# Performance work log

Hardware: AMD Instinct MI355X
Metric: run time of the kernel (lower is better)

Reference implementation:

```python
import jax, jax.numpy as jnp
import numpy as np

B, C, H, W = 2, 256, 64, 64
NH = 4          # num_heads -> ch = C // NH = 64
G = 32          # GroupNorm groups (normalization(channels))
EPS = 1e-5


def setup_inputs() -> dict:
    key = jax.random.key(0)
    ks = jax.random.split(key, 7)
    s = 1.0 / np.sqrt(C).astype(np.float32)
    return {
        "x": jax.random.normal(ks[0], (B, C, H, W), jnp.float32),
        "gn_scale": 1.0 + 0.02 * jax.random.normal(ks[1], (C,), jnp.float32),
        "gn_bias": 0.02 * jax.random.normal(ks[2], (C,), jnp.float32),
        "w_qkv": s * jax.random.normal(ks[3], (3 * C, C), jnp.float32),
        "b_qkv": jnp.zeros((3 * C,), jnp.float32),
        # NOTE: original zero-inits proj_out; we use random weights so the
        # attention path contributes to the output (meaningful baseline).
        "w_proj": s * jax.random.normal(ks[4], (C, C), jnp.float32),
        "b_proj": jnp.zeros((C,), jnp.float32),
    }


def reference(x, gn_scale, gn_bias, w_qkv, b_qkv, w_proj, b_proj):
    b, c = x.shape[0], x.shape[1]
    spatial = x.shape[2:]
    t = int(np.prod(spatial))
    xf = x.reshape(b, c, t)                      # [B, C, T]

    # GroupNorm(32) over (channels-in-group, T)
    xg = xf.reshape(b, G, c // G, t)
    mu = xg.mean(axis=(2, 3), keepdims=True)
    var = xg.var(axis=(2, 3), keepdims=True)
    xn = ((xg - mu) * jax.lax.rsqrt(var + EPS)).reshape(b, c, t)
    xn = xn * gn_scale[None, :, None] + gn_bias[None, :, None]

    # 1x1 conv -> qkv: [B, 3C, T]
    qkv = jnp.einsum('oc,bct->bot', w_qkv, xn) + b_qkv[None, :, None]

    # QKVAttentionLegacy: reshape (B*H, 3*ch, T) then split
    ch = c // NH
    qkv_h = qkv.reshape(b * NH, 3 * ch, t)
    q, k, v = jnp.split(qkv_h, 3, axis=1)        # each [B*H, ch, T]
    scale = 1.0 / np.sqrt(np.sqrt(ch)).astype(np.float32)
    w = jnp.einsum('bct,bcs->bts', q * scale, k * scale)   # [B*H, T, T]
    w = jax.nn.softmax(w.astype(jnp.float32), axis=-1).astype(qkv.dtype)
    a = jnp.einsum('bts,bcs->bct', w, v).reshape(b, c, t)  # [B, C, T]

    # proj 1x1 conv + residual
    h = jnp.einsum('oc,bct->bot', w_proj, a) + b_proj[None, :, None]
    return (xf + h).reshape(b, c, *spatial)
```

## Files before the change

### kernel.cpp

```cpp
#include <hip/hip_runtime.h>
#include <math.h>

#define T 4096
#define C 256
#define BATCH 2
#define NH 4
#define G 32
#define CPG 8
#define EPS 1e-5f
#define LOG2E 1.4426950408889634f
#define QSCALE (0.125f * LOG2E)
#define KSPLIT 4
#define KRANGE (T / KSPLIT)
#define KTILE 128
#define NIT (KRANGE / KTILE)
#define BH (BATCH * NH)

typedef __attribute__((ext_vector_type(8))) short bfv8;
typedef __attribute__((ext_vector_type(4))) short bfv4;
typedef __attribute__((ext_vector_type(4))) float f32x4;
typedef __attribute__((ext_vector_type(2))) float f32x2;
typedef __attribute__((ext_vector_type(16))) float f32x16;

static __device__ __forceinline__ short f2bf(float f) {
    union { float f; unsigned u; } v; v.f = f;
    return (short)((v.u + 0x7FFFu + ((v.u >> 16) & 1u)) >> 16);
}
static __device__ __forceinline__ float bf2f(short s) {
    union { float f; unsigned u; } v; v.u = ((unsigned)(unsigned short)s) << 16;
    return v.f;
}

#if __has_builtin(__builtin_amdgcn_exp2f)
#define EXP2(x) __builtin_amdgcn_exp2f(x)
#else
#define EXP2(x) exp2f(x)
#endif

#define AS1 __attribute__((address_space(1)))
#define AS3 __attribute__((address_space(3)))
static __device__ __forceinline__ void gll16(const void* g, void* l) {
    __builtin_amdgcn_global_load_lds((const AS1 void*)g, (AS3 void*)l, 16, 0, 0);
}

__global__ __launch_bounds__(256) void prep_stats(
    const float* __restrict__ wq, const float* __restrict__ wp,
    short* __restrict__ wqb, short* __restrict__ wpb,
    const float* __restrict__ x, float* __restrict__ gnp)
{
    __shared__ float rs[256], rss[256];
    const int bid = blockIdx.x;
    const int tid = threadIdx.x;
    if (bid < 256) {
        int i = bid * 256 + tid;
        const int NQ = 768 * 256 / 4;
        float4 v; short* dst;
        if (i < NQ) { v = ((const float4*)wq)[i]; dst = wqb + i * 4; }
        else        { int j = i - NQ; v = ((const float4*)wp)[j]; dst = wpb + j * 4; }
        bfv4 o = { f2bf(v.x), f2bf(v.y), f2bf(v.z), f2bf(v.w) };
        *(bfv4*)dst = o;
        return;
    }
    const int blk = (bid - 256) >> 2;
    const int ts  = (bid - 256) & 3;
    const int b = blk / G, g = blk % G;
    const float* xp = x + ((size_t)b * C + g * CPG) * T + ts * 1024;

    float s = 0.f, ss = 0.f;
    #pragma unroll
    for (int u = 0; u < CPG; u++) {
        float4 v = ((const float4*)(xp + (size_t)u * T))[tid];
        s  += v.x + v.y + v.z + v.w;
        ss += v.x*v.x + v.y*v.y + v.z*v.z + v.w*v.w;
    }
    rs[tid] = s; rss[tid] = ss;
    __syncthreads();
    for (int off = 128; off > 0; off >>= 1) {
        if (tid < off) { rs[tid] += rs[tid+off]; rss[tid] += rss[tid+off]; }
        __syncthreads();
    }
    if (tid == 0) {
        gnp[(blk * 4 + ts) * 2 + 0] = rs[0];
        gnp[(blk * 4 + ts) * 2 + 1] = rss[0];
    }
}

__global__ __launch_bounds__(256) void gn_norm(const float* __restrict__ x,
                                               const float* __restrict__ scale,
                                               const float* __restrict__ bias,
                                               const float* __restrict__ gnp,
                                               short* __restrict__ xnT) {
    const int blk = blockIdx.x;
    const int ts  = blockIdx.y;
    const int b = blk / G, g = blk % G;
    const int c0 = g * CPG;
    const float* xp = x + ((size_t)b * C + c0) * T;

    float s = 0.f, ss = 0.f;
    #pragma unroll
    for (int i = 0; i < 4; i++) {
        s  += gnp[(blk * 4 + i) * 2 + 0];
        ss += gnp[(blk * 4 + i) * 2 + 1];
    }
    const float inv_n = 1.0f / (CPG * T);
    const float mu  = s * inv_n;
    const float var = ss * inv_n - mu * mu;
    const float rstd = rsqrtf(var + EPS);

    float sc[CPG], bi[CPG];
    #pragma unroll
    for (int u = 0; u < CPG; u++) {
        sc[u] = scale[c0+u] * rstd;
        bi[u] = bias[c0+u] - mu * sc[u];
    }

    const int t = ts * 1024 + threadIdx.x * 4;
    float vv[CPG][4];
    #pragma unroll
    for (int u = 0; u < CPG; u++) {
        float4 v = *(const float4*)&xp[(size_t)u * T + t];
        vv[u][0] = v.x * sc[u] + bi[u];
        vv[u][1] = v.y * sc[u] + bi[u];
        vv[u][2] = v.z * sc[u] + bi[u];
        vv[u][3] = v.w * sc[u] + bi[u];
    }
    #pragma unroll
    for (int j = 0; j < 4; j++) {
        bfv8 w = { f2bf(vv[0][j]), f2bf(vv[1][j]), f2bf(vv[2][j]), f2bf(vv[3][j]),
                   f2bf(vv[4][j]), f2bf(vv[5][j]), f2bf(vv[6][j]), f2bf(vv[7][j]) };
        *(bfv8*)&xnT[((size_t)b * T + t + j) * C + c0] = w;
    }
}

__global__ __launch_bounds__(256) void gemm_qkv(
    const short* __restrict__ wq,
    const float* __restrict__ bq,
    const short* __restrict__ xnT,
    short* __restrict__ qb, short* __restrict__ kb, short* __restrict__ vb)
{
    const int b  = blockIdx.z;
    const int t0 = blockIdx.x * 64;
    const int ot = blockIdx.y;
    const int h = ot / 3, part = ot % 3;
    const int o0 = ot * 64;

    __shared__ short sm[8192];
    short* Ab = sm;
    short* Bb = sm + 4096;

    const int tid = threadIdx.x, lane = tid & 63, wave = tid >> 6;
    const int col = lane & 15, quad = lane >> 4;
    const short* xb = xnT + (size_t)b * T * C;

    f32x4 acc[4];
    #pragma unroll
    for (int g = 0; g < 4; g++) { acc[g][0]=0.f; acc[g][1]=0.f; acc[g][2]=0.f; acc[g][3]=0.f; }

    for (int k0 = 0; k0 < C; k0 += 64) {
        __syncthreads();
        #pragma unroll
        for (int hh = 0; hh < 2; hh++) {
            gll16(wq + (size_t)(o0 + 16*wave + col) * C + k0 + hh*32 + quad*8,
                  Ab + (hh*4 + wave) * 512);
            gll16(xb + (size_t)(t0 + 16*wave + col) * C + k0 + hh*32 + quad*8,
                  Bb + (hh*4 + wave) * 512);
        }
        __syncthreads();
        #pragma unroll
        for (int hh = 0; hh < 2; hh++) {
            bfv8 af = *(const bfv8*)(Ab + (hh*4 + wave) * 512 + lane*8);
            #pragma unroll
            for (int g = 0; g < 4; g++) {
                bfv8 bf = *(const bfv8*)(Bb + (hh*4 + g) * 512 + lane*8);
                acc[g] = __builtin_amdgcn_mfma_f32_16x16x32_bf16(af, bf, acc[g], 0, 0, 0);
            }
        }
    }

    const int olocal = 16*wave + quad*4;
    float bias_r[4];
    #pragma unroll
    for (int r = 0; r < 4; r++) bias_r[r] = bq[o0 + olocal + r];
    const size_t hd = (size_t)(b * NH + h);

    if (part < 2) {
        short* dst = (part == 0 ? qb : kb) + hd * T * 64;
        const float sc = (part == 0) ? QSCALE : 1.0f;
        #pragma unroll
        for (int g = 0; g < 4; g++) {
            int t = t0 + 16*g + col;
            bfv4 w = { f2bf((acc[g][0] + bias_r[0]) * sc),
                       f2bf((acc[g][1] + bias_r[1]) * sc),
                       f2bf((acc[g][2] + bias_r[2]) * sc),
                       f2bf((acc[g][3] + bias_r[3]) * sc) };
            *(bfv4*)&dst[(size_t)t * 64 + olocal] = w;
        }
    } else {
        short* dst = vb + hd * 64 * T;
        const int pcol = (col & 3) | ((col & 4) << 1) | ((col & 8) >> 1);
        #pragma unroll
        for (int g = 0; g < 4; g++)
            #pragma unroll
            for (int r = 0; r < 4; r++)
                dst[(size_t)(olocal + r) * T + t0 + 16*g + pcol] =
                    f2bf(acc[g][r] + bias_r[r]);
    }
}

__global__ __launch_bounds__(512, 4) void attn_kernel(
    const short* __restrict__ qb,
    const short* __restrict__ kb,
    const short* __restrict__ vb,
    short* __restrict__ opart,
    float* __restrict__ lp)
{
    __shared__ short smem[32768];
    const int flat = blockIdx.x;
    const int bh = flat & 7;
    const int tb = (flat >> 3) & 15;
    const int ks = flat >> 7;
    const int t0 = tb * 256;
    const int k0base = ks * KRANGE;
    const short* kbh = kb + (size_t)bh * T * 64;
    const short* vbh = vb + (size_t)bh * 64 * T;

    const int tid  = threadIdx.x;
    const int lane = tid & 63;
    const int wave = tid >> 6;
    const int klow = lane & 31;
    const int hi   = lane >> 5;

    const int q = t0 + wave*32 + klow;
    const short* qrow = qb + (size_t)bh * T * 64 + (size_t)q * 64;
    bfv8 qf[4];
    #pragma unroll
    for (int s = 0; s < 4; s++) qf[s] = *(const bfv8*)(qrow + s*16 + hi*8);

    f32x16 oacc[2];
    #pragma unroll
    for (int c = 0; c < 2; c++)
        #pragma unroll
        for (int r = 0; r < 16; r++) oacc[c][r] = 0.f;
    f32x2 l2 = { 0.f, 0.f };

    const int n1 = tid, n2 = tid + 512;
    const int kOff1 = ((n1>>8)*32 + (n1&31))*64 + ((n1>>6)&3)*16 + ((n1>>5)&1)*8;
    const int kOff2 = ((n2>>8)*32 + (n2&31))*64 + ((n2>>6)&3)*16 + ((n2>>5)&1)*8;
    const size_t vRow1 = (size_t)(((n1>>9)<<5) + (n1&31)) * T;
    const size_t vRow2 = (size_t)(((n2>>9)<<5) + (n2&31)) * T;
    const int vCol1 = ((n1>>6)&7)*16 + ((n1>>5)&1)*8;
    const int vCol2 = ((n2>>6)&7)*16 + ((n2>>5)&1)*8;
    #define STAGE_KV(buf, s0)                                                   \
        {                                                                       \
            short* base = smem + (buf) * 16384;                                 \
            gll16(kbh + (size_t)(s0) * 64 + kOff1, base + n1*8);                \
            gll16(kbh + (size_t)(s0) * 64 + kOff2, base + n2*8);                \
            gll16(vbh + vRow1 + (s0) + vCol1, base + 8192 + n1*8);              \
            gll16(vbh + vRow2 + (s0) + vCol2, base + 8192 + n2*8);              \
        }

    STAGE_KV(0, k0base)

    for (int it = 0; it < NIT; it++) {
        __syncthreads();
        if (it + 1 < NIT) STAGE_KV((it+1) & 1, k0base + (it+1)*KTILE)

        const short* kvb = smem + (it & 1) * 16384;

        #pragma unroll
        for (int kt = 0; kt < 4; kt++) {
            f32x16 sacc;
            #pragma unroll
            for (int r = 0; r < 16; r++) sacc[r] = 0.f;
            #pragma unroll
            for (int s = 0; s < 4; s++) {
                bfv8 kf = *(const bfv8*)(kvb + ((kt*4 + s)*64 + lane)*8);
                sacc = __builtin_amdgcn_mfma_f32_32x32x16_bf16(kf, qf[s], sacc, 0, 0, 0);
            }
            #pragma unroll
            for (int u = 0; u < 2; u++) {
                float p[8];
                #pragma unroll
                for (int j = 0; j < 8; j++) p[j] = EXP2(sacc[8*u + j]);
                f32x2 pa = { p[0], p[1] }, pb = { p[2], p[3] };
                f32x2 pc = { p[4], p[5] }, pd = { p[6], p[7] };
                l2 += (pa + pb) + (pc + pd);
                union { unsigned w[4]; bfv8 v; } pk_;
                #pragma unroll
                for (int w = 0; w < 4; w++)
                    asm("v_cvt_pk_bf16_f32 %0, %1, %2"
                        : "=v"(pk_.w[w]) : "v"(p[2*w]), "v"(p[2*w+1]));
                const int kc = 2*kt + u;
                #pragma unroll
                for (int c = 0; c < 2; c++) {
                    bfv8 vf = *(const bfv8*)(kvb + 8192 + ((c*8 + kc)*64 + lane)*8);
                    oacc[c] = __builtin_amdgcn_mfma_f32_32x32x16_bf16(
                                  vf, pk_.v, oacc[c], 0, 0, 0);
                }
            }
        }
    }

    float lsum = l2[0] + l2[1];
    lsum += __shfl_xor(lsum, 32);

    const size_t rowbase = (size_t)(ks*BH + bh) * T + t0 + wave*32;
    short* opb = opart + (rowbase + klow) * 64;
    #pragma unroll
    for (int c = 0; c < 2; c++)
        #pragma unroll
        for (int u = 0; u < 4; u++) {
            bfv4 w = { f2bf(oacc[c][4*u+0]), f2bf(oacc[c][4*u+1]),
                       f2bf(oacc[c][4*u+2]), f2bf(oacc[c][4*u+3]) };
            *(bfv4*)(opb + c*32 + u*8 + hi*4) = w;
        }
    if (hi == 0) {
        lp[rowbase + klow] = lsum;
    }
}

__global__ __launch_bounds__(256) void gemm_proj(
    const short* __restrict__ wp,
    const float* __restrict__ bp,
    const short* __restrict__ opart,
    const float* __restrict__ lp,
    const float* __restrict__ x,
    float* __restrict__ out)
{
    const int b  = blockIdx.z;
    const int t0 = blockIdx.x * 64;
    const int o0 = blockIdx.y * 64;

    __shared__ short sm[8192];
    short* Ab = sm;
    short* Bb = sm + 4096;

    const int tid = threadIdx.x, lane = tid & 63, wave = tid >> 6;
    const int col = lane & 15, quad = lane >> 4;

    const int trow = t0 + 16*wave + col;
    float rl4[NH];
    #pragma unroll
    for (int hh = 0; hh < NH; hh++) {
        float ls = 0.f;
        #pragma unroll
        for (int ks = 0; ks < KSPLIT; ks++)
            ls += lp[((size_t)(ks*BH) + b*NH + hh) * T + trow];
        rl4[hh] = 1.0f / ls;
    }

    f32x4 acc[4];
    #pragma unroll
    for (int g = 0; g < 4; g++) { acc[g][0]=0.f; acc[g][1]=0.f; acc[g][2]=0.f; acc[g][3]=0.f; }

    for (int k0 = 0; k0 < C; k0 += 64) {
        __syncthreads();
        #pragma unroll
        for (int hh = 0; hh < 2; hh++) {
            gll16(wp + (size_t)(o0 + 16*wave + col) * C + k0 + hh*32 + quad*8,
                  Ab + (hh*4 + wave) * 512);
            const int chg = k0 + hh*32 + quad*8;
            const int hd = chg >> 6, chin = chg & 63;
            const short* ob = opart + (((size_t)(b*NH + hd)) * T + trow) * 64 + chin;
            float a8[8] = {0.f,0.f,0.f,0.f,0.f,0.f,0.f,0.f};
            #pragma unroll
            for (int ks = 0; ks < KSPLIT; ks++) {
                bfv8 v = *(const bfv8*)(ob + (size_t)ks * BH * T * 64);
                #pragma unroll
                for (int u = 0; u < 8; u++) a8[u] += bf2f(v[u]);
            }
            const float rl = rl4[hd];
            bfv8 pk;
            #pragma unroll
            for (int u = 0; u < 8; u++) pk[u] = f2bf(a8[u] * rl);
            *(bfv8*)(Bb + (hh*4 + wave) * 512 + lane*8) = pk;
        }
        __syncthreads();
        #pragma unroll
        for (int hh = 0; hh < 2; hh++) {
            bfv8 af = *(const bfv8*)(Ab + (hh*4 + wave) * 512 + lane*8);
            #pragma unroll
            for (int g = 0; g < 4; g++) {
                bfv8 bf = *(const bfv8*)(Bb + (hh*4 + g) * 512 + lane*8);
                acc[g] = __builtin_amdgcn_mfma_f32_16x16x32_bf16(af, bf, acc[g], 0, 0, 0);
            }
        }
    }

    const int olocal = 16*wave + quad*4;
    #pragma unroll
    for (int r = 0; r < 4; r++) {
        const int o = o0 + olocal + r;
        const float bias = bp[o];
        const size_t rowoff = ((size_t)b * C + o) * T;
        #pragma unroll
        for (int g = 0; g < 4; g++) {
            const size_t idx = rowoff + t0 + 16*g + col;
            out[idx] = acc[g][r] + bias + x[idx];
        }
    }
}

extern "C" void kernel_launch(void* const* d_in, const int* in_sizes, int n_in,
                              void* d_out, int out_size, void* d_ws, size_t ws_size,
                              hipStream_t stream) {
    (void)in_sizes; (void)n_in; (void)out_size; (void)ws_size;
    const float* x        = (const float*)d_in[0];
    const float* gn_scale = (const float*)d_in[1];
    const float* gn_bias  = (const float*)d_in[2];
    const float* w_qkv    = (const float*)d_in[3];
    const float* b_qkv    = (const float*)d_in[4];
    const float* w_proj   = (const float*)d_in[5];
    const float* b_proj   = (const float*)d_in[6];
    float* out = (float*)d_out;

    short* ws    = (short*)d_ws;
    short* qb    = ws;
    short* kb    = qb  + (size_t)BH * T * 64;
    short* vb    = kb  + (size_t)BH * T * 64;
    short* xnT   = vb  + (size_t)BH * T * 64;
    short* wqb   = xnT + (size_t)BATCH * T * C;
    short* wpb   = wqb + 768 * 256;
    short* opart = wpb + 256 * 256;
    float* lp    = (float*)(opart + (size_t)KSPLIT * BH * T * 64);
    float* gnp   = lp + (size_t)KSPLIT * BH * T;

    prep_stats<<<dim3(512), 256, 0, stream>>>(w_qkv, w_proj, wqb, wpb, x, gnp);
    gn_norm<<<dim3(BATCH * G, 4), 256, 0, stream>>>(x, gn_scale, gn_bias, gnp, xnT);
    gemm_qkv<<<dim3(T/64, 12, BATCH), 256, 0, stream>>>(wqb, b_qkv, xnT, qb, kb, vb);
    attn_kernel<<<dim3(512), 512, 0, stream>>>(qb, kb, vb, opart, lp);
    gemm_proj<<<dim3(T/64, 4, BATCH), 256, 0, stream>>>(wpb, b_proj, opart, lp, x, out);
}
```

Measured before the change: 146.8 us.

## Give each attention wave two query tiles to reuse K/V fragments

The attention kernel moves from 8 waves of 32 queries each to 4 waves of 64 queries each. Each wave now holds two query tiles, so every K and V fragment read from LDS feeds two MFMAs instead of one. The KV tile shrinks to 64 keys and LDS use is halved. The aim is to cut LDS read traffic per MFMA, at the cost of doubled accumulator registers, a lower occupancy bound, and more barrier iterations per block.

Measured after the change: 146.6 us. No clear change (-0.1%).

```diff
diff --git a/kernel.cpp b/kernel.cpp
--- a/kernel.cpp
+++ b/kernel.cpp
@@ -12,7 +12,7 @@
 #define QSCALE (0.125f * LOG2E)
 #define KSPLIT 4
 #define KRANGE (T / KSPLIT)
-#define KTILE 128
+#define KTILE 64
 #define NIT (KRANGE / KTILE)
 #define BH (BATCH * NH)
 
@@ -207,14 +207,14 @@
     }
 }
 
-__global__ __launch_bounds__(512, 4) void attn_kernel(
+__global__ __launch_bounds__(256, 2) void attn_kernel(
     const short* __restrict__ qb,
     const short* __restrict__ kb,
     const short* __restrict__ vb,
     short* __restrict__ opart,
     float* __restrict__ lp)
 {
-    __shared__ short smem[32768];
+    __shared__ short smem[16384];
     const int flat = blockIdx.x;
     const int bh = flat & 7;
     const int tb = (flat >> 3) & 15;
@@ -230,33 +230,37 @@
     const int klow = lane & 31;
     const int hi   = lane >> 5;
 
-    const int q = t0 + wave*32 + klow;
-    const short* qrow = qb + (size_t)bh * T * 64 + (size_t)q * 64;
-    bfv8 qf[4];
-    #pragma unroll
-    for (int s = 0; s < 4; s++) qf[s] = *(const bfv8*)(qrow + s*16 + hi*8);
-
-    f32x16 oacc[2];
+    const short* qrowA = qb + (size_t)bh * T * 64
+                            + (size_t)(t0 + wave*64 + klow) * 64;
+    const short* qrowB = qrowA + (size_t)32 * 64;
+    bfv8 qfA[4], qfB[4];
+    #pragma unroll
+    for (int s = 0; s < 4; s++) {
+        qfA[s] = *(const bfv8*)(qrowA + s*16 + hi*8);
+        qfB[s] = *(const bfv8*)(qrowB + s*16 + hi*8);
+    }
+
+    f32x16 oaccA[2], oaccB[2];
     #pragma unroll
     for (int c = 0; c < 2; c++)
         #pragma unroll
-        for (int r = 0; r < 16; r++) oacc[c][r] = 0.f;
-    f32x2 l2 = { 0.f, 0.f };
-
-    const int n1 = tid, n2 = tid + 512;
+        for (int r = 0; r < 16; r++) { oaccA[c][r] = 0.f; oaccB[c][r] = 0.f; }
+    f32x2 l2A = { 0.f, 0.f }, l2B = { 0.f, 0.f };
+
+    const int n1 = tid, n2 = tid + 256;
     const int kOff1 = ((n1>>8)*32 + (n1&31))*64 + ((n1>>6)&3)*16 + ((n1>>5)&1)*8;
     const int kOff2 = ((n2>>8)*32 + (n2&31))*64 + ((n2>>6)&3)*16 + ((n2>>5)&1)*8;
-    const size_t vRow1 = (size_t)(((n1>>9)<<5) + (n1&31)) * T;
-    const size_t vRow2 = (size_t)(((n2>>9)<<5) + (n2&31)) * T;
-    const int vCol1 = ((n1>>6)&7)*16 + ((n1>>5)&1)*8;
-    const int vCol2 = ((n2>>6)&7)*16 + ((n2>>5)&1)*8;
+    const size_t vRow1 = (size_t)((n1>>8)*32 + (n1&31)) * T;
+    const size_t vRow2 = (size_t)((n2>>8)*32 + (n2&31)) * T;
+    const int vCol1 = ((n1>>6)&3)*16 + ((n1>>5)&1)*8;
+    const int vCol2 = ((n2>>6)&3)*16 + ((n2>>5)&1)*8;
     #define STAGE_KV(buf, s0)                                                   \
         {                                                                       \
-            short* base = smem + (buf) * 16384;                                 \
+            short* base = smem + (buf) * 8192;                                  \
             gll16(kbh + (size_t)(s0) * 64 + kOff1, base + n1*8);                \
             gll16(kbh + (size_t)(s0) * 64 + kOff2, base + n2*8);                \
-            gll16(vbh + vRow1 + (s0) + vCol1, base + 8192 + n1*8);              \
-            gll16(vbh + vRow2 + (s0) + vCol2, base + 8192 + n2*8);              \
+            gll16(vbh + vRow1 + (s0) + vCol1, base + 4096 + n1*8);              \
+            gll16(vbh + vRow2 + (s0) + vCol2, base + 4096 + n2*8);              \
         }
 
     STAGE_KV(0, k0base)
@@ -265,57 +269,76 @@
         __syncthreads();
         if (it + 1 < NIT) STAGE_KV((it+1) & 1, k0base + (it+1)*KTILE)
 
-        const short* kvb = smem + (it & 1) * 16384;
-
-        #pragma unroll
-        for (int kt = 0; kt < 4; kt++) {
-            f32x16 sacc;
-            #pragma unroll
-            for (int r = 0; r < 16; r++) sacc[r] = 0.f;
+        const short* kvb = smem + (it & 1) * 8192;
+
+        #pragma unroll
+        for (int kt = 0; kt < 2; kt++) {
+            f32x16 sA, sB;
+            #pragma unroll
+            for (int r = 0; r < 16; r++) { sA[r] = 0.f; sB[r] = 0.f; }
             #pragma unroll
             for (int s = 0; s < 4; s++) {
                 bfv8 kf = *(const bfv8*)(kvb + ((kt*4 + s)*64 + lane)*8);
-                sacc = __builtin_amdgcn_mfma_f32_32x32x16_bf16(kf, qf[s], sacc, 0, 0, 0);
+                sA = __builtin_amdgcn_mfma_f32_32x32x16_bf16(kf, qfA[s], sA, 0, 0, 0);
+                sB = __builtin_amdgcn_mfma_f32_32x32x16_bf16(kf, qfB[s], sB, 0, 0, 0);
             }
             #pragma unroll
             for (int u = 0; u < 2; u++) {
-                float p[8];
+                float pA[8], pB[8];
                 #pragma unroll
-                for (int j = 0; j < 8; j++) p[j] = EXP2(sacc[8*u + j]);
-                f32x2 pa = { p[0], p[1] }, pb = { p[2], p[3] };
-                f32x2 pc = { p[4], p[5] }, pd = { p[6], p[7] };
-                l2 += (pa + pb) + (pc + pd);
-                union { unsigned w[4]; bfv8 v; } pk_;
+                for (int j = 0; j < 8; j++) {
+                    pA[j] = EXP2(sA[8*u + j]);
+                    pB[j] = EXP2(sB[8*u + j]);
+                }
+                f32x2 a0 = { pA[0], pA[1] }, a1 = { pA[2], pA[3] };
+                f32x2 a2 = { pA[4], pA[5] }, a3 = { pA[6], pA[7] };
+                l2A += (a0 + a1) + (a2 + a3);
+                f32x2 b0 = { pB[0], pB[1] }, b1 = { pB[2], pB[3] };
+                f32x2 b2 = { pB[4], pB[5] }, b3 = { pB[6], pB[7] };
+                l2B += (b0 + b1) + (b2 + b3);
+                union { unsigned w[4]; bfv8 v; } pkA_, pkB_;
                 #pragma unroll
-                for (int w = 0; w < 4; w++)
+                for (int w = 0; w < 4; w++) {
                     asm("v_cvt_pk_bf16_f32 %0, %1, %2"
-                        : "=v"(pk_.w[w]) : "v"(p[2*w]), "v"(p[2*w+1]));
+                        : "=v"(pkA_.w[w]) : "v"(pA[2*w]), "v"(pA[2*w+1]));
+                    asm("v_cvt_pk_bf16_f32 %0, %1, %2"
+                        : "=v"(pkB_.w[w]) : "v"(pB[2*w]), "v"(pB[2*w+1]));
+                }
                 const int kc = 2*kt + u;
                 #pragma unroll
                 for (int c = 0; c < 2; c++) {
-                    bfv8 vf = *(const bfv8*)(kvb + 8192 + ((c*8 + kc)*64 + lane)*8);
-                    oacc[c] = __builtin_amdgcn_mfma_f32_32x32x16_bf16(
-                                  vf, pk_.v, oacc[c], 0, 0, 0);
+                    bfv8 vf = *(const bfv8*)(kvb + 4096 + ((c*4 + kc)*64 + lane)*8);
+                    oaccA[c] = __builtin_amdgcn_mfma_f32_32x32x16_bf16(
+                                   vf, pkA_.v, oaccA[c], 0, 0, 0);
+                    oaccB[c] = __builtin_amdgcn_mfma_f32_32x32x16_bf16(
+                                   vf, pkB_.v, oaccB[c], 0, 0, 0);
                 }
             }
         }
     }
 
-    float lsum = l2[0] + l2[1];
-    lsum += __shfl_xor(lsum, 32);
-
-    const size_t rowbase = (size_t)(ks*BH + bh) * T + t0 + wave*32;
-    short* opb = opart + (rowbase + klow) * 64;
+    float lsumA = l2A[0] + l2A[1];
+    float lsumB = l2B[0] + l2B[1];
+    lsumA += __shfl_xor(lsumA, 32);
+    lsumB += __shfl_xor(lsumB, 32);
+
+    const size_t rowbase = (size_t)(ks*BH + bh) * T + t0 + wave*64;
+    short* opbA = opart + (rowbase + klow) * 64;
+    short* opbB = opart + (rowbase + 32 + klow) * 64;
     #pragma unroll
     for (int c = 0; c < 2; c++)
         #pragma unroll
         for (int u = 0; u < 4; u++) {
-            bfv4 w = { f2bf(oacc[c][4*u+0]), f2bf(oacc[c][4*u+1]),
-                       f2bf(oacc[c][4*u+2]), f2bf(oacc[c][4*u+3]) };
-            *(bfv4*)(opb + c*32 + u*8 + hi*4) = w;
+            bfv4 wA = { f2bf(oaccA[c][4*u+0]), f2bf(oaccA[c][4*u+1]),
+                        f2bf(oaccA[c][4*u+2]), f2bf(oaccA[c][4*u+3]) };
+            *(bfv4*)(opbA + c*32 + u*8 + hi*4) = wA;
+            bfv4 wB = { f2bf(oaccB[c][4*u+0]), f2bf(oaccB[c][4*u+1]),
+                        f2bf(oaccB[c][4*u+2]), f2bf(oaccB[c][4*u+3]) };
+            *(bfv4*)(opbB + c*32 + u*8 + hi*4) = wB;
         }
     if (hi == 0) {
-        lp[rowbase + klow] = lsum;
+        lp[rowbase + klow] = lsumA;
+        lp[rowbase + 32 + klow] = lsumB;
     }
 }
 
@@ -428,6 +451,6 @@
     prep_stats<<<dim3(512), 256, 0, stream>>>(w_qkv, w_proj, wqb, wpb, x, gnp);
     gn_norm<<<dim3(BATCH * G, 4), 256, 0, stream>>>(x, gn_scale, gn_bias, gnp, xnT);
     gemm_qkv<<<dim3(T/64, 12, BATCH), 256, 0, stream>>>(wqb, b_qkv, xnT, qb, kb, vb);
-    attn_kernel<<<dim3(512), 512, 0, stream>>>(qb, kb, vb, opart, lp);
+    attn_kernel<<<dim3(512), 256, 0, stream>>>(qb, kb, vb, opart, lp);
     gemm_proj<<<dim3(T/64, 4, BATCH), 256, 0, stream>>>(wpb, b_proj, opart, lp, x, out);
 }
```

## Load K/V fragments directly from global memory instead of LDS double-buffering

Applied to the files above, without the earlier changes.

Drops the shared-memory double-buffered staging of K and V tiles (async global-to-LDS loads plus a block barrier per tile) in the attention kernel. Each wave now reads its K and V MFMA fragments straight from global memory and relies on the L1/L2 caches for reuse across the block's eight waves. It also relaxes the launch bounds from a minimum of 4 blocks per CU to none. This removes LDS traffic and barrier stalls, but it makes every wave reissue the same global loads. Load latency is no longer hidden by the explicit prefetch, and occupancy may change with the looser register bound.

Measured after the change: 229.5 us. 1.56x slower.

```diff
diff --git a/kernel.cpp b/kernel.cpp
--- a/kernel.cpp
+++ b/kernel.cpp
@@ -12,8 +12,6 @@
 #define QSCALE (0.125f * LOG2E)
 #define KSPLIT 4
 #define KRANGE (T / KSPLIT)
-#define KTILE 128
-#define NIT (KRANGE / KTILE)
 #define BH (BATCH * NH)
 
 typedef __attribute__((ext_vector_type(8))) short bfv8;
@@ -207,14 +205,13 @@
     }
 }
 
-__global__ __launch_bounds__(512, 4) void attn_kernel(
+__global__ __launch_bounds__(512) void attn_kernel(
     const short* __restrict__ qb,
     const short* __restrict__ kb,
     const short* __restrict__ vb,
     short* __restrict__ opart,
     float* __restrict__ lp)
 {
-    __shared__ short smem[32768];
     const int flat = blockIdx.x;
     const int bh = flat & 7;
     const int tb = (flat >> 3) & 15;
@@ -243,61 +240,40 @@
         for (int r = 0; r < 16; r++) oacc[c][r] = 0.f;
     f32x2 l2 = { 0.f, 0.f };
 
-    const int n1 = tid, n2 = tid + 512;
-    const int kOff1 = ((n1>>8)*32 + (n1&31))*64 + ((n1>>6)&3)*16 + ((n1>>5)&1)*8;
-    const int kOff2 = ((n2>>8)*32 + (n2&31))*64 + ((n2>>6)&3)*16 + ((n2>>5)&1)*8;
-    const size_t vRow1 = (size_t)(((n1>>9)<<5) + (n1&31)) * T;
-    const size_t vRow2 = (size_t)(((n2>>9)<<5) + (n2&31)) * T;
-    const int vCol1 = ((n1>>6)&7)*16 + ((n1>>5)&1)*8;
-    const int vCol2 = ((n2>>6)&7)*16 + ((n2>>5)&1)*8;
-    #define STAGE_KV(buf, s0)                                                   \
-        {                                                                       \
-            short* base = smem + (buf) * 16384;                                 \
-            gll16(kbh + (size_t)(s0) * 64 + kOff1, base + n1*8);                \
-            gll16(kbh + (size_t)(s0) * 64 + kOff2, base + n2*8);                \
-            gll16(vbh + vRow1 + (s0) + vCol1, base + 8192 + n1*8);              \
-            gll16(vbh + vRow2 + (s0) + vCol2, base + 8192 + n2*8);              \
-        }
-
-    STAGE_KV(0, k0base)
-
-    for (int it = 0; it < NIT; it++) {
-        __syncthreads();
-        if (it + 1 < NIT) STAGE_KV((it+1) & 1, k0base + (it+1)*KTILE)
-
-        const short* kvb = smem + (it & 1) * 16384;
-
-        #pragma unroll
-        for (int kt = 0; kt < 4; kt++) {
-            f32x16 sacc;
-            #pragma unroll
-            for (int r = 0; r < 16; r++) sacc[r] = 0.f;
-            #pragma unroll
-            for (int s = 0; s < 4; s++) {
-                bfv8 kf = *(const bfv8*)(kvb + ((kt*4 + s)*64 + lane)*8);
-                sacc = __builtin_amdgcn_mfma_f32_32x32x16_bf16(kf, qf[s], sacc, 0, 0, 0);
-            }
-            #pragma unroll
-            for (int u = 0; u < 2; u++) {
-                float p[8];
-                #pragma unroll
-                for (int j = 0; j < 8; j++) p[j] = EXP2(sacc[8*u + j]);
-                f32x2 pa = { p[0], p[1] }, pb = { p[2], p[3] };
-                f32x2 pc = { p[4], p[5] }, pd = { p[6], p[7] };
-                l2 += (pa + pb) + (pc + pd);
-                union { unsigned w[4]; bfv8 v; } pk_;
-                #pragma unroll
-                for (int w = 0; w < 4; w++)
-                    asm("v_cvt_pk_bf16_f32 %0, %1, %2"
-                        : "=v"(pk_.w[w]) : "v"(p[2*w]), "v"(p[2*w+1]));
-                const int kc = 2*kt + u;
-                #pragma unroll
-                for (int c = 0; c < 2; c++) {
-                    bfv8 vf = *(const bfv8*)(kvb + 8192 + ((c*8 + kc)*64 + lane)*8);
-                    oacc[c] = __builtin_amdgcn_mfma_f32_32x32x16_bf16(
-                                  vf, pk_.v, oacc[c], 0, 0, 0);
-                }
-            }
+    const short* krow  = kbh + (size_t)(k0base + klow) * 64 + hi*8;
+    const short* vrow0 = vbh + (size_t)klow * T        + k0base + hi*8;
+    const short* vrow1 = vbh + (size_t)(32 + klow) * T + k0base + hi*8;
+
+    #pragma unroll 4
+    for (int kt = 0; kt < KRANGE/32; kt++) {
+        const short* kp = krow + kt*2048;
+        f32x16 sacc;
+        #pragma unroll
+        for (int r = 0; r < 16; r++) sacc[r] = 0.f;
+        #pragma unroll
+        for (int s = 0; s < 4; s++) {
+            bfv8 kf = *(const bfv8*)(kp + s*16);
+            sacc = __builtin_amdgcn_mfma_f32_32x32x16_bf16(kf, qf[s], sacc, 0, 0, 0);
+        }
+        #pragma unroll
+        for (int u = 0; u < 2; u++) {
+            float p[8];
+            #pragma unroll
+            for (int j = 0; j < 8; j++) p[j] = EXP2(sacc[8*u + j]);
+            f32x2 pa = { p[0], p[1] }, pb = { p[2], p[3] };
+            f32x2 pc = { p[4], p[5] }, pd = { p[6], p[7] };
+            l2 += (pa + pb) + (pc + pd);
+            union { unsigned w[4]; bfv8 v; } pk_;
+            #pragma unroll
+            for (int w = 0; w < 4; w++)
+                asm("v_cvt_pk_bf16_f32 %0, %1, %2"
+                    : "=v"(pk_.w[w]) : "v"(p[2*w]), "v"(p[2*w+1]));
+            bfv8 vf0 = *(const bfv8*)(vrow0 + kt*32 + u*16);
+            bfv8 vf1 = *(const bfv8*)(vrow1 + kt*32 + u*16);
+            oacc[0] = __builtin_amdgcn_mfma_f32_32x32x16_bf16(
+                          vf0, pk_.v, oacc[0], 0, 0, 0);
+            oacc[1] = __builtin_amdgcn_mfma_f32_32x32x16_bf16(
+                          vf1, pk_.v, oacc[1], 0, 0, 0);
         }
     }
 
```
